# Optimization experiments

Measured on AMD Instinct MI355X. Metric: run time of the kernel, lower is better.

## Reference

```python
import jax, jax.numpy as jnp
from jax import lax
import numpy as np

B, CIN, COUT, WDIM, RES = 8, 512, 512, 512, 64


def setup_inputs() -> dict:
    key = jax.random.key(0)
    k0, k1, k2, k3 = jax.random.split(key, 4)
    x = jax.random.normal(k0, (B, CIN, RES, RES), dtype=jnp.float32)
    w = jax.random.normal(k1, (B, WDIM), dtype=jnp.float32)
    weight = jax.random.normal(k2, (COUT, CIN, 3, 3), dtype=jnp.float32)
    bias = jnp.zeros((COUT,), dtype=jnp.float32)
    affine_w = jax.random.normal(k3, (CIN, WDIM), dtype=jnp.float32) * 0.02
    affine_b = jnp.zeros((CIN,), dtype=jnp.float32)
    return {"x": x, "w": w, "weight": weight, "bias": bias,
            "affine_w": affine_w, "affine_b": affine_b}


def reference(x, w, weight, bias, affine_w, affine_b):
    # style: [B, Cin] = affine(w)
    style = w @ affine_w.T + affine_b
    b, cin, h, wd = x.shape
    cout = weight.shape[0]
    # per-sample modulated weight: [B, Cout, Cin, 3, 3]
    wmod = weight[None, :, :, :, :] * style[:, None, :, None, None]
    # grouped conv with groups = batch: lhs [1, B*Cin, H, W], rhs [B*Cout, Cin, 3, 3]
    lhs = x.reshape(1, b * cin, h, wd)
    rhs = wmod.reshape(b * cout, cin, 3, 3)
    y = lax.conv_general_dilated(
        lhs, rhs,
        window_strides=(1, 1),
        padding=[(1, 1), (1, 1)],
        dimension_numbers=("NCHW", "OIHW", "NCHW"),
        feature_group_count=b,
    )
    y = y.reshape(b, cout, h, wd)
    return y + bias[None, :, None, None]
```

## Files before the change

### kernel.cpp

```cpp
#include <hip/hip_runtime.h>
#include <cstdint>
#include <cstddef>

#define BATCH 8
#define CIN   512
#define COUT  512
#define RES   64
#define HW    4096
#define WDIM  512

typedef short bf16x8 __attribute__((ext_vector_type(8)));
typedef float f32x4  __attribute__((ext_vector_type(4)));
typedef unsigned short ushort8 __attribute__((ext_vector_type(8)));

typedef const __attribute__((address_space(1))) void* gas_ptr;
typedef __attribute__((address_space(3))) void*       las_ptr;

__device__ __forceinline__ unsigned short f2bf(float f) {
    unsigned int u = __float_as_uint(f);
    u += 0x7fffu + ((u >> 16) & 1u);
    return (unsigned short)(u >> 16);
}

__global__ __launch_bounds__(256) void prep_kernel(
    const float* __restrict__ w, const float* __restrict__ aw,
    const float* __restrict__ ab, float* __restrict__ style,
    unsigned short* __restrict__ zpage,
    const float* __restrict__ wt, unsigned short* __restrict__ wr)
{
    __shared__ float buf[4608];
    int bid = blockIdx.x;
    int t = threadIdx.x;
    if (bid < 1024) {
        if (bid == 0 && t < 128) zpage[t] = 0;
        int wv = t >> 6, lane = t & 63;
        int idx = bid * 4 + wv;
        int b = idx >> 9, ci = idx & 511;
        const float* wrow = w + b * WDIM;
        const float* arow = aw + (size_t)ci * WDIM;
        float s = 0.f;
#pragma unroll
        for (int i = 0; i < WDIM / 64; ++i) s += arow[lane + i * 64] * wrow[lane + i * 64];
#pragma unroll
        for (int off = 32; off; off >>= 1) s += __shfl_down(s, off);
        if (lane == 0) style[idx] = s + ab[ci];
    } else {
        int co = bid - 1024;
#pragma unroll
        for (int r = 0; r < 18; ++r) buf[r * 256 + t] = wt[(size_t)co * 4608 + r * 256 + t];
        __syncthreads();
#pragma unroll
        for (int r = 0; r < 18; ++r) {
            int idx = r * 256 + t;
            int tap = idx >> 9, ci = idx & 511;
            wr[(size_t)tap * (COUT * CIN) + co * CIN + ci] = f2bf(buf[ci * 9 + tap]);
        }
    }
}

__global__ __launch_bounds__(256) void modtrans_kernel(
    const float* __restrict__ x, const float* __restrict__ style,
    unsigned short* __restrict__ xs)
{
    __shared__ float tile[64][65];
    int t = threadIdx.x;
    int hw0 = blockIdx.x * 64, ci0 = blockIdx.y * 64, b = blockIdx.z;
    int sub = t >> 6, lane = t & 63;
#pragma unroll
    for (int r = 0; r < 16; ++r) {
        int ci = r * 4 + sub;
        float s = style[b * CIN + ci0 + ci];
        tile[ci][lane] = x[((size_t)(b * CIN + ci0 + ci)) * HW + hw0 + lane] * s;
    }
    __syncthreads();
    int ci8 = (t & 7) * 8;
#pragma unroll
    for (int r = 0; r < 2; ++r) {
        int hw = r * 32 + (t >> 3);
        ushort8 v;
#pragma unroll
        for (int j = 0; j < 8; ++j) v[j] = f2bf(tile[ci8 + j][hw]);
        *(ushort8*)&xs[((size_t)b * HW + hw0 + hw) * CIN + ci0 + ci8] = v;
    }
}

__global__ __launch_bounds__(512, 2) void conv_kernel(
    const unsigned short* __restrict__ xs,
    const unsigned short* __restrict__ wr,
    const float* __restrict__ bias,
    const unsigned short* __restrict__ zpage,
    float* __restrict__ y)
{
    __shared__ __align__(16) unsigned short As[2 * 3 * 256 * 32];
    __shared__ __align__(16) unsigned short Bs[2 * 4 * 66 * 32];
    constexpr int ABUF = 3 * 256 * 32;
    constexpr int BBUF = 4 * 66 * 32;

    const int t   = threadIdx.x;
    const int bid = blockIdx.x;
    const int b    = bid & 7;
    const int hgrp = (bid >> 3) & 15;
    const int co0  = (bid >> 7) * 256;
    const int h0   = hgrp * 4;

    const int lane = t & 63;
    const int wv   = t >> 6;
    const int wm   = (wv & 1) * 128;
    const int wn   = (wv >> 1) * 64;
    const int r16  = lane & 15;
    const int quad = lane >> 4;

    {
        int bufz = t >> 8;
        int r = t & 255;
        int d = r >> 6, c = r & 63;
        int col = (c < 32) ? 0 : 65;
        Bs[bufz * BBUF + (d * 66 + col) * 32 + (c & 31)] = 0;
    }

    f32x4 acc[8][4];
#pragma unroll
    for (int mi = 0; mi < 8; ++mi)
#pragma unroll
        for (int ni = 0; ni < 4; ++ni)
            acc[mi][ni] = (f32x4){0.f, 0.f, 0.f, 0.f};

    const unsigned short* pA[6];
    const unsigned short* pB[2];
    int sB[2];

    auto setup = [&](int kh) {
#pragma unroll
        for (int L = 0; L < 6; ++L) {
            int lin = L * 512 + t;
            int tap = kh * 3 + (lin >> 10);
            int q   = (lin >> 2) & 255;
            int c8  = ((lin & 3) ^ ((lin >> 3) & 3)) * 8;
            pA[L] = wr + (size_t)tap * (COUT * CIN) + (co0 + q) * CIN + c8;
        }
#pragma unroll
        for (int L = 0; L < 2; ++L) {
            int lin = L * 512 + t;
            int dh = lin >> 8, r8 = lin & 255;
            int wc = r8 >> 2;
            int rowp = dh * 66 + 1 + wc;
            int c8 = ((r8 & 3) ^ ((rowp >> 1) & 3)) * 8;
            int hp = h0 + dh + kh - 1;
            bool ok = (unsigned)hp < 64u;
            pB[L] = ok ? xs + ((size_t)b * HW + hp * 64 + wc) * CIN + c8 : zpage;
            sB[L] = ok ? 32 : 0;
        }
    };

    auto stage = [&](int buf) {
        const int ab = buf * ABUF, bb = buf * BBUF;
#pragma unroll
        for (int L = 0; L < 6; ++L) {
            int lin = L * 512 + t;
            __builtin_amdgcn_global_load_lds((gas_ptr)pA[L], (las_ptr)&As[ab + lin * 8], 16, 0, 0);
            pA[L] += 32;
        }
#pragma unroll
        for (int L = 0; L < 2; ++L) {
            int lin = L * 512 + t;
            int dh = lin >> 8, r8 = lin & 255;
            __builtin_amdgcn_global_load_lds((gas_ptr)pB[L],
                (las_ptr)&Bs[bb + (dh * 66 + 1) * 32 + r8 * 8], 16, 0, 0);
            pB[L] += sB[L];
        }
    };

    setup(0);
    stage(0);

    for (int p = 0; p < 48; ++p) {
        __syncthreads();

        if (p < 47) {
            int pn = p + 1;
            if ((pn & 15) == 0) setup(pn >> 4);
            stage(pn & 1);
        }
        __builtin_amdgcn_sched_barrier(0);

        const int ab = (p & 1) * ABUF, bb = (p & 1) * BBUF;
#pragma unroll
        for (int kw = 0; kw < 3; ++kw) {
            bf16x8 af[8], bfv[4];
#pragma unroll
            for (int mi = 0; mi < 8; ++mi) {
                int row = kw * 256 + wm + mi * 16 + r16;
                int ck  = quad ^ ((row >> 1) & 3);
                af[mi] = *(const bf16x8*)&As[ab + row * 32 + ck * 8];
            }
#pragma unroll
            for (int ni = 0; ni < 4; ++ni) {
                int n = wn + ni * 16 + r16;
                int dh = n >> 6, wc = n & 63;
                int row = dh * 66 + wc + kw;
                int ck  = quad ^ ((row >> 1) & 3);
                bfv[ni] = *(const bf16x8*)&Bs[bb + row * 32 + ck * 8];
            }
            __builtin_amdgcn_s_setprio(1);
#pragma unroll
            for (int mi = 0; mi < 8; ++mi)
#pragma unroll
                for (int ni = 0; ni < 4; ++ni)
                    acc[mi][ni] = __builtin_amdgcn_mfma_f32_16x16x32_bf16(
                        af[mi], bfv[ni], acc[mi][ni], 0, 0, 0);
            __builtin_amdgcn_s_setprio(0);
        }
    }

    const size_t hw0 = (size_t)hgrp * 256;
#pragma unroll
    for (int mi = 0; mi < 8; ++mi) {
#pragma unroll
        for (int r = 0; r < 4; ++r) {
            int m = co0 + wm + mi * 16 + quad * 4 + r;
            float bv = bias[m];
            size_t base = ((size_t)b * COUT + m) * HW + hw0;
#pragma unroll
            for (int ni = 0; ni < 4; ++ni) {
                int n = wn + ni * 16 + r16;
                y[base + n] = acc[mi][ni][r] + bv;
            }
        }
    }
}

extern "C" void kernel_launch(void* const* d_in, const int* in_sizes, int n_in,
                              void* d_out, int out_size, void* d_ws, size_t ws_size,
                              hipStream_t stream)
{
    (void)in_sizes; (void)n_in; (void)out_size; (void)ws_size;
    const float* x    = (const float*)d_in[0];
    const float* w    = (const float*)d_in[1];
    const float* wt   = (const float*)d_in[2];
    const float* bias = (const float*)d_in[3];
    const float* aw   = (const float*)d_in[4];
    const float* ab   = (const float*)d_in[5];
    float* y = (float*)d_out;

    char* ws = (char*)d_ws;
    float*          style = (float*)ws;
    unsigned short* zpage = (unsigned short*)(ws + 16384);
    unsigned short* wr    = (unsigned short*)(ws + 32768);
    unsigned short* xs    = (unsigned short*)(ws + 4751360);

    prep_kernel<<<1536, 256, 0, stream>>>(w, aw, ab, style, zpage, wt, wr);
    modtrans_kernel<<<dim3(64, 8, 8), 256, 0, stream>>>(x, style, xs);
    conv_kernel<<<256, 512, 0, stream>>>(xs, wr, bias, zpage, y);
}
```

Before: 252.7 us.

## Load weight fragments directly from global memory instead of staging in LDS

Result: slower. 416.7 us (+64.9%).

```diff
diff --git a/kernel.cpp b/kernel.cpp
--- a/kernel.cpp
+++ b/kernel.cpp
@@ -91,9 +91,7 @@
     const unsigned short* __restrict__ zpage,
     float* __restrict__ y)
 {
-    __shared__ __align__(16) unsigned short As[2 * 3 * 256 * 32];
     __shared__ __align__(16) unsigned short Bs[2 * 4 * 66 * 32];
-    constexpr int ABUF = 3 * 256 * 32;
     constexpr int BBUF = 4 * 66 * 32;
 
     const int t   = threadIdx.x;
@@ -110,6 +108,8 @@
     const int r16  = lane & 15;
     const int quad = lane >> 4;
 
+    const size_t awoff = (size_t)(co0 + wm + r16) * CIN + quad * 8;
+
     {
         int bufz = t >> 8;
         int r = t & 255;
@@ -125,19 +125,10 @@
         for (int ni = 0; ni < 4; ++ni)
             acc[mi][ni] = (f32x4){0.f, 0.f, 0.f, 0.f};
 
-    const unsigned short* pA[6];
     const unsigned short* pB[2];
     int sB[2];
 
-    auto setup = [&](int kh) {
-#pragma unroll
-        for (int L = 0; L < 6; ++L) {
-            int lin = L * 512 + t;
-            int tap = kh * 3 + (lin >> 10);
-            int q   = (lin >> 2) & 255;
-            int c8  = ((lin & 3) ^ ((lin >> 3) & 3)) * 8;
-            pA[L] = wr + (size_t)tap * (COUT * CIN) + (co0 + q) * CIN + c8;
-        }
+    auto setupB = [&](int kh) {
 #pragma unroll
         for (int L = 0; L < 2; ++L) {
             int lin = L * 512 + t;
@@ -152,14 +143,8 @@
         }
     };
 
-    auto stage = [&](int buf) {
-        const int ab = buf * ABUF, bb = buf * BBUF;
-#pragma unroll
-        for (int L = 0; L < 6; ++L) {
-            int lin = L * 512 + t;
-            __builtin_amdgcn_global_load_lds((gas_ptr)pA[L], (las_ptr)&As[ab + lin * 8], 16, 0, 0);
-            pA[L] += 32;
-        }
+    auto stageB = [&](int buf) {
+        const int bb = buf * BBUF;
 #pragma unroll
         for (int L = 0; L < 2; ++L) {
             int lin = L * 512 + t;
@@ -170,29 +155,31 @@
         }
     };
 
-    setup(0);
-    stage(0);
+    setupB(0);
+    stageB(0);
 
     for (int p = 0; p < 48; ++p) {
+        const int kh = p >> 4;
+        const int ci0 = (p & 15) * 32;
+
         __syncthreads();
 
         if (p < 47) {
             int pn = p + 1;
-            if ((pn & 15) == 0) setup(pn >> 4);
-            stage(pn & 1);
-        }
-        __builtin_amdgcn_sched_barrier(0);
-
-        const int ab = (p & 1) * ABUF, bb = (p & 1) * BBUF;
+            if ((pn & 15) == 0) setupB(pn >> 4);
+            stageB(pn & 1);
+        }
+
+        const int bb = (p & 1) * BBUF;
 #pragma unroll
         for (int kw = 0; kw < 3; ++kw) {
+            const int tap = kh * 3 + kw;
+            const unsigned short* pa = wr + (size_t)tap * (COUT * CIN) + awoff + ci0;
+
             bf16x8 af[8], bfv[4];
 #pragma unroll
-            for (int mi = 0; mi < 8; ++mi) {
-                int row = kw * 256 + wm + mi * 16 + r16;
-                int ck  = quad ^ ((row >> 1) & 3);
-                af[mi] = *(const bf16x8*)&As[ab + row * 32 + ck * 8];
-            }
+            for (int mi = 0; mi < 8; ++mi)
+                af[mi] = *(const bf16x8*)(pa + (size_t)mi * 16 * CIN);
 #pragma unroll
             for (int ni = 0; ni < 4; ++ni) {
                 int n = wn + ni * 16 + r16;
```
